# Kernel optimization log

Hardware: AMD Instinct MI355X
Metric: run time of the kernel (lower is better)

Reference implementation:

```python
import jax, jax.numpy as jnp
import numpy as np

N_HEAD, D_HEAD, D_MODEL = 16, 64, 1024
QLEN, MEMLEN, BSZ = 1024, 1024, 2
KLEN = QLEN + MEMLEN  # rlen == klen
LN_EPS = 1e-5
NEG = -1e30


def _rel_shift(x):
    # x: [qlen, rlen, bsz, n_head] -> Transformer-XL relative shift
    q, r, b, n = x.shape
    zp = jnp.zeros((q, 1, b, n), x.dtype)
    xp = jnp.concatenate([zp, x], axis=1).reshape(r + 1, q, b, n)
    return xp[1:].reshape(q, r, b, n)


def _layer_norm(x, gamma, beta):
    mu = jnp.mean(x, axis=-1, keepdims=True)
    var = jnp.mean((x - mu) ** 2, axis=-1, keepdims=True)
    return (x - mu) * jax.lax.rsqrt(var + LN_EPS) * gamma + beta


def setup_inputs() -> dict:
    key = jax.random.key(0)
    ks = jax.random.split(key, 8)
    w = jax.random.normal(ks[0], (QLEN, BSZ, D_MODEL), jnp.float32)
    r = jax.random.normal(ks[1], (KLEN, D_MODEL), jnp.float32)
    r_w_bias = jax.random.normal(ks[2], (N_HEAD, D_HEAD), jnp.float32) * 0.02
    r_r_bias = jax.random.normal(ks[3], (N_HEAD, D_HEAD), jnp.float32) * 0.02
    mems = jax.random.normal(ks[4], (MEMLEN, BSZ, D_MODEL), jnp.float32)
    W_qkv = jax.random.normal(ks[5], (D_MODEL, 3 * N_HEAD * D_HEAD), jnp.float32) * 0.02
    W_r = jax.random.normal(ks[6], (D_MODEL, N_HEAD * D_HEAD), jnp.float32) * 0.02
    W_o = jax.random.normal(ks[7], (N_HEAD * D_HEAD, D_MODEL), jnp.float32) * 0.02
    ln_gamma = jnp.ones((D_MODEL,), jnp.float32)
    ln_beta = jnp.zeros((D_MODEL,), jnp.float32)
    # causal mask with memory: key j visible to query i iff j <= i + MEMLEN (True = keep)
    attn_mask = jnp.arange(KLEN)[None, :] <= (jnp.arange(QLEN)[:, None] + MEMLEN)
    return {"w": w, "r": r, "r_w_bias": r_w_bias, "r_r_bias": r_r_bias,
            "mems": mems, "attn_mask": attn_mask, "W_qkv": W_qkv, "W_r": W_r,
            "W_o": W_o, "ln_gamma": ln_gamma, "ln_beta": ln_beta}


def reference(w, r, r_w_bias, r_r_bias, mems, attn_mask, W_qkv, W_r, W_o, ln_gamma, ln_beta):
    qlen, bsz = w.shape[0], w.shape[1]
    scale = 1.0 / (D_HEAD ** 0.5)
    cat = jnp.concatenate([mems, w], axis=0)            # [klen, b, d_model]
    klen = cat.shape[0]
    w_heads = cat @ W_qkv                                # [klen, b, 3*H*D]
    r_head_k = (r @ W_r).reshape(-1, N_HEAD, D_HEAD)     # [rlen, H, D]
    w_head_q, w_head_k, w_head_v = jnp.split(w_heads, 3, axis=-1)
    w_head_q = w_head_q[-qlen:].reshape(qlen, bsz, N_HEAD, D_HEAD)
    w_head_k = w_head_k.reshape(klen, bsz, N_HEAD, D_HEAD)
    w_head_v = w_head_v.reshape(klen, bsz, N_HEAD, D_HEAD)
    AC = jnp.einsum('ibnd,jbnd->ijbn', w_head_q + r_w_bias, w_head_k)
    BD = jnp.einsum('ibnd,jnd->ijbn', w_head_q + r_r_bias, r_head_k)
    BD = _rel_shift(BD)
    attn_score = (AC + BD) * scale                       # [q, k, b, n]
    attn_score = jnp.where(attn_mask[:, :, None, None], attn_score, NEG)
    attn_prob = jax.nn.softmax(attn_score, axis=1)
    attn_vec = jnp.einsum('ijbn,jbnd->ibnd', attn_prob, w_head_v)
    attn_vec = attn_vec.reshape(qlen, bsz, N_HEAD * D_HEAD)
    attn_out = attn_vec @ W_o                            # [q, b, d_model]
    return _layer_norm(w + attn_out, ln_gamma, ln_beta)
```

## Files before the change

kernel.cpp:

```cpp
#include <hip/hip_runtime.h>
#include <hip/hip_bf16.h>

#define NHEAD 16
#define DHEAD 64
#define DMODEL 1024
#define QLEN 1024
#define MEMLEN 1024
#define BSZ 2
#define KLEN 2048
#define LN_EPS 1e-5f

typedef __hip_bfloat16 bf16;
typedef __attribute__((ext_vector_type(8))) short short8;
typedef __attribute__((ext_vector_type(4))) float f32x4;

__device__ __forceinline__ float b2f(bf16 x) { return __bfloat162float(x); }
__device__ __forceinline__ bf16 f2b(float x) { return __float2bfloat16(x); }
__device__ __forceinline__ short f2bs(float f) {
    bf16 h = __float2bfloat16(f);
    return *reinterpret_cast<short*>(&h);
}
__device__ __forceinline__ float s2f(short s) {
    bf16 h = *reinterpret_cast<bf16*>(&s);
    return __bfloat162float(h);
}
__device__ __forceinline__ float fexp2(float x) {
    float y;
    asm("v_exp_f32 %0, %1" : "=v"(y) : "v"(x));
    return y;
}

#define MFMA16(a, b, c) __builtin_amdgcn_mfma_f32_16x16x32_bf16(a, b, c, 0, 0, 0)

#define AS1 __attribute__((address_space(1)))
#define AS3 __attribute__((address_space(3)))
__device__ __forceinline__ void gld16(const bf16* g, bf16* l) {
    __builtin_amdgcn_global_load_lds((const AS1 void*)(uintptr_t)g,
                                     (AS3 void*)(uint32_t)(uintptr_t)l, 16, 0, 0);
}

__global__ __launch_bounds__(256)
void prep(const float* __restrict__ mems, const float* __restrict__ w,
          const float* __restrict__ r, const float* __restrict__ Wqkv,
          const float* __restrict__ Wr, const float* __restrict__ Wo,
          bf16* __restrict__ Abf, bf16* __restrict__ rbf,
          bf16* __restrict__ Wqkvt, bf16* __restrict__ Wrt,
          bf16* __restrict__ Wot) {
    __shared__ bf16 T[64][65];
    const int id = blockIdx.x;
    const int t = threadIdx.x;
    if (id < 6144) {
        const float* src;
        bf16* dst;
        int off;
        if (id < 2048)      { src = mems; dst = Abf;                       off = id; }
        else if (id < 4096) { src = w;    dst = Abf + (size_t)2048 * 1024; off = id - 2048; }
        else                { src = r;    dst = rbf;                       off = id - 4096; }
        int i = off * 256 + t;
        const float4 v = reinterpret_cast<const float4*>(src)[i];
        bf16 o[4] = {f2b(v.x), f2b(v.y), f2b(v.z), f2b(v.w)};
        reinterpret_cast<ulong1*>(dst)[i] = *reinterpret_cast<ulong1*>(o);
        return;
    }
    int tid2 = id - 6144;
    const float* in;
    bf16* out;
    int N, tn, tile;
    if (tid2 < 768)       { in = Wqkv; out = Wqkvt; N = 3072; tn = 48; tile = tid2; }
    else if (tid2 < 1024) { in = Wr;   out = Wrt;   N = 1024; tn = 16; tile = tid2 - 768; }
    else                  { in = Wo;   out = Wot;   N = 1024; tn = 16; tile = tid2 - 1024; }
    const int K = 1024;
    const int n0 = (tile % tn) * 64, k0 = (tile / tn) * 64;
    #pragma unroll
    for (int e = 0; e < 16; e++) {
        int flat = e * 256 + t;
        int kl = flat >> 6, nl = flat & 63;
        T[kl][nl] = f2b(in[(size_t)(k0 + kl) * N + n0 + nl]);
    }
    __syncthreads();
    #pragma unroll
    for (int e = 0; e < 16; e++) {
        int flat = e * 256 + t;
        int nl = flat >> 6, kl = flat & 63;
        out[(size_t)(n0 + nl) * K + k0 + kl] = T[kl][nl];
    }
}

__global__ __launch_bounds__(256)
void gemm_mfma(const bf16* __restrict__ A, const bf16* __restrict__ Bt,
               const bf16* __restrict__ A2, const bf16* __restrict__ B2,
               int M, int N, int K, int mode,
               const float* __restrict__ rwb, const float* __restrict__ rrb,
               bf16* __restrict__ Qw, bf16* __restrict__ Qr,
               bf16* __restrict__ Kb, bf16* __restrict__ Vt,
               bf16* __restrict__ Cb, float* __restrict__ Cf,
               float* __restrict__ Cf2) {
    const int bm = blockIdx.x * 128, bn = blockIdx.y * 128;
    int sub = 0;
    const bf16* Ap = A;
    const bf16* Bp = Bt;
    if (mode == 0 && bm < 2048 && bn < 1024) { sub = 1; Ap = A2; Bp = B2; }
    const int ldk = (mode == 2) ? 1024 : K;
    float* Cfz = Cf;
    if (mode == 2 && blockIdx.z) { Ap += 512; Bp += 512; Cfz = Cf2; }
    __shared__ bf16 As[128 * 64];
    __shared__ bf16 Bs[128 * 64];
    const int t = threadIdx.x;
    const int w = t >> 6, lane = t & 63, quad = lane >> 4, l16 = lane & 15;
    const int wm = (w >> 1) * 64, wn = (w & 1) * 64;
    const int srow = lane >> 3;
    const int scs = ((lane & 7) ^ srow) * 8;
    const int c0 = (quad ^ (l16 & 7)) * 8;

    f32x4 acc[4][4];
    #pragma unroll
    for (int mt = 0; mt < 4; mt++)
        #pragma unroll
        for (int nt = 0; nt < 4; nt++) acc[mt][nt] = (f32x4){0.f, 0.f, 0.f, 0.f};

    for (int k0 = 0; k0 < K; k0 += 64) {
        #pragma unroll
        for (int e = 0; e < 4; e++) {
            int ch = w + 4 * e;
            int row = ch * 8 + srow;
            gld16(Ap + (size_t)(bm + row) * ldk + k0 + scs, As + ch * 512);
            gld16(Bp + (size_t)(bn + row) * ldk + k0 + scs, Bs + ch * 512);
        }
        __syncthreads();
        #pragma unroll
        for (int kk = 0; kk < 2; kk++) {
            const int cc = c0 ^ (kk << 5);
            short8 af[4], bfr[4];
            #pragma unroll
            for (int mt = 0; mt < 4; mt++)
                af[mt] = *reinterpret_cast<short8*>(&As[(wm + 16 * mt + l16) * 64 + cc]);
            #pragma unroll
            for (int nt = 0; nt < 4; nt++)
                bfr[nt] = *reinterpret_cast<short8*>(&Bs[(wn + 16 * nt + l16) * 64 + cc]);
            #pragma unroll
            for (int mt = 0; mt < 4; mt++)
                #pragma unroll
                for (int nt = 0; nt < 4; nt++)
                    acc[mt][nt] = MFMA16(af[mt], bfr[nt], acc[mt][nt]);
        }
        __syncthreads();
    }

    const float QSC = 0.18033688f;
    #pragma unroll
    for (int mt = 0; mt < 4; mt++)
        #pragma unroll
        for (int nt = 0; nt < 4; nt++)
            #pragma unroll
            for (int r = 0; r < 4; r++) {
                int m = bm + wm + 16 * mt + quad * 4 + r;
                int c = bn + wn + 16 * nt + l16;
                float v = acc[mt][nt][r];
                if (sub) {
                    Cb[(size_t)m * 1024 + c] = f2b(v);
                } else if (mode == 0) {
                    int seg = c >> 10, cc2 = c & 1023;
                    if (seg == 0) {
                        if (m >= 2048) {
                            size_t o = (size_t)(m - 2048) * 1024 + cc2;
                            Qw[o] = f2b((v + rwb[cc2]) * QSC);
                            Qr[o] = f2b((v + rrb[cc2]) * QSC);
                        }
                    } else if (seg == 1) {
                        Kb[(size_t)m * 1024 + cc2] = f2b(v);
                    } else {
                        Vt[((size_t)cc2 * 2 + (m & 1)) * 2048 + (m >> 1)] = f2b(v);
                    }
                } else {
                    Cfz[(size_t)m * N + c] = v;
                }
            }
}

__global__ __launch_bounds__(256, 3)
void attn_mfma(const bf16* __restrict__ Qw, const bf16* __restrict__ Qr,
               const bf16* __restrict__ Kb, const bf16* __restrict__ Vt,
               const bf16* __restrict__ Rk, float* __restrict__ O0g,
               float* __restrict__ O1g, float2* __restrict__ ML) {
    const int id = blockIdx.x;
    const int xcd = id & 7, local = id >> 3;
    const int pidx = local & 3;
    const int couple = (local >> 2) & 7;
    const int chunk = local >> 5;
    const int pair = xcd * 4 + pidx;
    const int b = pair & 1, n = pair >> 1;
    const int TA = couple + 17;
    const int t_beg = (chunk == 0) ? 0 : (chunk == 1) ? 17 : 33;
    const int t_end = (chunk == 0) ? 17 : (chunk == 1) ? 33 : 49;

    int segs[2][4];
    int nseg = 0;
    {
        int aend = min(t_end, TA);
        if (t_beg < aend) {
            segs[nseg][0] = couple; segs[nseg][1] = t_beg;
            segs[nseg][2] = aend;   segs[nseg][3] = (t_beg == 0) ? 0 : 1;
            nseg++;
        }
        int bbeg = max(t_beg, TA);
        if (bbeg < t_end) {
            segs[nseg][0] = 15 - couple; segs[nseg][1] = bbeg - TA;
            segs[nseg][2] = t_end - TA;  segs[nseg][3] = (bbeg == TA) ? 0 : 1;
            nseg++;
        }
    }

    const int tid = threadIdx.x;
    const int w = tid >> 6, lane = tid & 63;
    const int quad = lane >> 4, l16 = lane & 15;
    const int ln8 = lane >> 3;
    const int cs = (lane & 7) ^ (ln8 & 7);
    const int q0 = (quad ^ (l16 & 7)) * 8;
    const int q1 = q0 ^ 32;
    const int rbl = 48 - 16 * w;

    __shared__ bf16 Ks[64 * 64];
    __shared__ bf16 Vs[64 * 64];
    __shared__ bf16 Rs[3][64 * 64];
    __shared__ short WP_s[4][16 * 82];
    short* WP = WP_s[w];

    const int koff = b * 1024 + n * 64 + cs * 8;
    const size_t voff = (size_t)n * 262144 + b * 2048 + cs * 8;
    const int rcol = n * 64 + cs * 8;

    for (int sg = 0; sg < nseg; sg++) {
        const int i0 = segs[sg][0], jb = segs[sg][1], je = segs[sg][2], slot = segs[sg][3];
        const int I0 = i0 * 64;
        const int qbase = I0 + 16 * w;
        const int RB = 960 - I0;
        const int jlast = i0 + 16;

        auto stageKV = [&](int tt) {
            const int J0t = tt * 64;
            #pragma unroll
            for (int e = 0; e < 2; e++) {
                int ch = w + 4 * e;
                gld16(Vt + (size_t)(ch * 8 + ln8) * 4096 + voff + J0t, Vs + ch * 512);
                gld16(Kb + (size_t)(J0t + ch * 8 + ln8) * 2048 + koff, Ks + ch * 512);
            }
        };
        auto stageR = [&](int u) {
            bf16* rd = Rs[u % 3];
            #pragma unroll
            for (int e = 0; e < 2; e++) {
                int ch = w + 4 * e;
                int rrow = min(RB + u * 64 + ch * 8 + ln8, 2047);
                gld16(Rk + (size_t)rrow * 1024 + rcol, rd + ch * 512);
            }
        };

        short8 aqw[2], aqr[2];
        {
            const bf16* qp = Qw + ((size_t)(qbase + l16) * 2 + b) * 1024 + n * 64 + quad * 8;
            aqw[0] = *reinterpret_cast<const short8*>(qp);
            aqw[1] = *reinterpret_cast<const short8*>(qp + 32);
            const bf16* qp2 = Qr + ((size_t)(qbase + l16) * 2 + b) * 1024 + n * 64 + quad * 8;
            aqr[0] = *reinterpret_cast<const short8*>(qp2);
            aqr[1] = *reinterpret_cast<const short8*>(qp2 + 32);
        }

        f32x4 O[4];
        #pragma unroll
        for (int d = 0; d < 4; d++) O[d] = (f32x4){0.f, 0.f, 0.f, 0.f};
        float m_run = -1e30f;
        float pl[4] = {0.f, 0.f, 0.f, 0.f};

        if (sg) {
            asm volatile("s_waitcnt vmcnt(0)" ::: "memory");
            __builtin_amdgcn_s_barrier();
        }
        stageR(jb); stageR(jb + 1);

        for (int j = jb; j < je; j++) {
            const int J0 = j * 64;

            asm volatile("s_waitcnt vmcnt(0)" ::: "memory");
            __builtin_amdgcn_s_barrier();

            stageKV(j);
            stageR(j + 2);

            const bf16* R0 = Rs[j % 3];
            const bf16* R1 = Rs[(j + 1) % 3];

            #pragma unroll
            for (int s = 0; s < 5; s++) {
                int rb2 = rbl + 16 * s;
                const bf16* Rb = (rb2 & 64) ? R1 : R0;
                int rh = (rb2 & 63) + l16;
                short8 b0 = *reinterpret_cast<const short8*>(&Rb[rh * 64 + q0]);
                short8 b1 = *reinterpret_cast<const short8*>(&Rb[rh * 64 + q1]);
                f32x4 acc = (f32x4){0.f, 0.f, 0.f, 0.f};
                __builtin_amdgcn_s_setprio(1);
                acc = MFMA16(aqr[0], b0, acc);
                acc = MFMA16(aqr[1], b1, acc);
                __builtin_amdgcn_s_setprio(0);
                #pragma unroll
                for (int r = 0; r < 4; r++)
                    WP[(quad * 4 + r) * 82 + 16 * s + l16] = f2bs(acc[r]);
            }

            asm volatile("s_waitcnt vmcnt(2)" ::: "memory");
            __builtin_amdgcn_s_barrier();

            float sv[4][4];
            #pragma unroll
            for (int n16 = 0; n16 < 4; n16++) {
                int kr = 16 * n16 + l16;
                short8 k0 = *reinterpret_cast<const short8*>(&Ks[kr * 64 + q0]);
                short8 k1 = *reinterpret_cast<const short8*>(&Ks[kr * 64 + q1]);
                f32x4 acc = (f32x4){0.f, 0.f, 0.f, 0.f};
                __builtin_amdgcn_s_setprio(1);
                acc = MFMA16(aqw[0], k0, acc);
                acc = MFMA16(aqw[1], k1, acc);
                __builtin_amdgcn_s_setprio(0);
                #pragma unroll
                for (int r = 0; r < 4; r++) {
                    int row = quad * 4 + r, col = 16 * n16 + l16;
                    sv[n16][r] = acc[r] + s2f(WP[row * 82 + col - row + 15]);
                }
            }
            if (j == jlast) {
                #pragma unroll
                for (int n16 = 0; n16 < 4; n16++)
                    #pragma unroll
                    for (int r = 0; r < 4; r++) {
                        int row = quad * 4 + r, col = 16 * n16 + l16;
                        if (J0 + col > qbase + row + MEMLEN) sv[n16][r] = -1e30f;
                    }
            }

            float mx = sv[0][0];
            #pragma unroll
            for (int n16 = 0; n16 < 4; n16++)
                #pragma unroll
                for (int r = 0; r < 4; r++) mx = fmaxf(mx, sv[n16][r]);
            #pragma unroll
            for (int msk = 1; msk < 16; msk <<= 1) mx = fmaxf(mx, __shfl_xor(mx, msk));
            if (mx > m_run + 11.5f) {
                const float alpha = fexp2(m_run - mx);
                m_run = mx;
                #pragma unroll
                for (int r = 0; r < 4; r++) pl[r] *= alpha;
                #pragma unroll
                for (int d = 0; d < 4; d++)
                    #pragma unroll
                    for (int r = 0; r < 4; r++) O[d][r] *= alpha;
            }
            #pragma unroll
            for (int n16 = 0; n16 < 4; n16++)
                #pragma unroll
                for (int r = 0; r < 4; r++) sv[n16][r] = fexp2(sv[n16][r] - m_run);
            #pragma unroll
            for (int r = 0; r < 4; r++)
                pl[r] += sv[0][r] + sv[1][r] + sv[2][r] + sv[3][r];

            #pragma unroll
            for (int n16 = 0; n16 < 4; n16++)
                #pragma unroll
                for (int r = 0; r < 4; r++)
                    WP[(quad * 4 + r) * 72 + 16 * n16 + l16] = f2bs(sv[n16][r]);
            short8 ap0 = *reinterpret_cast<short8*>(&WP[l16 * 72 + quad * 8]);
            short8 ap1 = *reinterpret_cast<short8*>(&WP[l16 * 72 + 32 + quad * 8]);

            __builtin_amdgcn_s_setprio(1);
            #pragma unroll
            for (int ds = 0; ds < 4; ds++) {
                int dr = 16 * ds + l16;
                short8 v0 = *reinterpret_cast<const short8*>(&Vs[dr * 64 + q0]);
                short8 v1 = *reinterpret_cast<const short8*>(&Vs[dr * 64 + q1]);
                O[ds] = MFMA16(ap0, v0, O[ds]);
                O[ds] = MFMA16(ap1, v1, O[ds]);
            }
            __builtin_amdgcn_s_setprio(0);
        }

        float lr[4];
        #pragma unroll
        for (int r = 0; r < 4; r++) {
            float s = pl[r];
            #pragma unroll
            for (int msk = 1; msk < 16; msk <<= 1) s += __shfl_xor(s, msk);
            lr[r] = s;
        }
        if (l16 == 0) {
            #pragma unroll
            for (int r = 0; r < 4; r++) {
                int q = qbase + quad * 4 + r;
                ML[(size_t)slot * 32768 + (q * 2 + b) * 16 + n] =
                    make_float2(m_run, lr[r]);
            }
        }
        float* Od = slot ? O1g : O0g;
        #pragma unroll
        for (int ds = 0; ds < 4; ds++)
            #pragma unroll
            for (int r = 0; r < 4; r++) {
                int q = qbase + quad * 4 + r;
                Od[((size_t)q * 2 + b) * 1024 + n * 64 + 16 * ds + l16] = O[ds][r];
            }
    }
}

__global__ __launch_bounds__(256)
void attn_combine(const float* __restrict__ O0, const float* __restrict__ O1,
                  const float2* __restrict__ ML, bf16* __restrict__ AVbf) {
    const int row = blockIdx.x;
    const int t = threadIdx.x;
    const int n = t >> 4;
    const int i0 = row >> 7;
    const float2 a0 = ML[row * 16 + n];
    const f32x4 p0 = reinterpret_cast<const f32x4*>(O0)[row * 256 + t];
    short o[4];
    if (i0 != 0) {
        const float2 a1 = ML[32768 + row * 16 + n];
        const float m = fmaxf(a0.x, a1.x);
        const float e0 = fexp2(a0.x - m);
        const float e1 = fexp2(a1.x - m);
        const float inv = 1.f / (a0.y * e0 + a1.y * e1);
        const f32x4 p1 = reinterpret_cast<const f32x4*>(O1)[row * 256 + t];
        #pragma unroll
        for (int jj = 0; jj < 4; jj++)
            o[jj] = f2bs((p0[jj] * e0 + p1[jj] * e1) * inv);
    } else {
        const float inv = 1.f / a0.y;
        #pragma unroll
        for (int jj = 0; jj < 4; jj++) o[jj] = f2bs(p0[jj] * inv);
    }
    reinterpret_cast<ulong1*>(AVbf)[row * 256 + t] = *reinterpret_cast<ulong1*>(o);
}

__global__ __launch_bounds__(256)
void ln_res(const float* __restrict__ ao0, const float* __restrict__ ao1,
            const float* __restrict__ w, const float* __restrict__ gamma,
            const float* __restrict__ beta, float* __restrict__ out) {
    const int m = blockIdx.x;
    const int t = threadIdx.x;
    const int wv = t >> 6, lane = t & 63;
    __shared__ float red[8];
    float x[4];
    #pragma unroll
    for (int e = 0; e < 4; e++) {
        int c = e * 256 + t;
        x[e] = ao0[(size_t)m * DMODEL + c] + ao1[(size_t)m * DMODEL + c]
             + w[(size_t)m * DMODEL + c];
    }
    float s = x[0] + x[1] + x[2] + x[3];
    #pragma unroll
    for (int msk = 1; msk < 64; msk <<= 1) s += __shfl_xor(s, msk);
    if (lane == 0) red[wv] = s;
    __syncthreads();
    const float mu = (red[0] + red[1] + red[2] + red[3]) * (1.f / 1024.f);
    float s2 = 0.f;
    #pragma unroll
    for (int e = 0; e < 4; e++) { float dx = x[e] - mu; s2 += dx * dx; }
    #pragma unroll
    for (int msk = 1; msk < 64; msk <<= 1) s2 += __shfl_xor(s2, msk);
    if (lane == 0) red[4 + wv] = s2;
    __syncthreads();
    const float rstd = rsqrtf((red[4] + red[5] + red[6] + red[7]) * (1.f / 1024.f) + LN_EPS);
    #pragma unroll
    for (int e = 0; e < 4; e++) {
        int c = e * 256 + t;
        out[(size_t)m * DMODEL + c] = (x[e] - mu) * rstd * gamma[c] + beta[c];
    }
}

extern "C" void kernel_launch(void* const* d_in, const int* in_sizes, int n_in,
                              void* d_out, int out_size, void* d_ws, size_t ws_size,
                              hipStream_t stream) {
    const float* w        = (const float*)d_in[0];
    const float* r        = (const float*)d_in[1];
    const float* r_w_bias = (const float*)d_in[2];
    const float* r_r_bias = (const float*)d_in[3];
    const float* mems     = (const float*)d_in[4];
    const float* W_qkv    = (const float*)d_in[6];
    const float* W_r      = (const float*)d_in[7];
    const float* W_o      = (const float*)d_in[8];
    const float* gamma    = (const float*)d_in[9];
    const float* beta     = (const float*)d_in[10];
    float* out = (float*)d_out;

    bf16* Abf    = (bf16*)d_ws;
    bf16* Wqkvt  = Abf   + (size_t)4096 * 1024;
    bf16* Wrt    = Wqkvt + (size_t)3072 * 1024;
    bf16* Wot    = Wrt   + (size_t)1024 * 1024;
    bf16* rbf    = Wot   + (size_t)1024 * 1024;
    bf16* Qw     = rbf   + (size_t)2048 * 1024;
    bf16* Qr     = Qw    + (size_t)2048 * 1024;
    bf16* Kb     = Qr    + (size_t)2048 * 1024;
    bf16* Vt     = Kb    + (size_t)4096 * 1024;
    bf16* Rk     = Vt    + (size_t)2048 * 2048;
    bf16* AVbf   = Rk    + (size_t)2048 * 1024;
    float* Opart0   = (float*)Abf;
    float* Opart1   = (float*)Wqkvt;
    float2* ML      = (float2*)rbf;
    float* attn_out0 = (float*)Abf;
    float* attn_out1 = (float*)Wqkvt;

    dim3 b256(256);
    prep<<<dim3(7424), b256, 0, stream>>>(mems, w, r, W_qkv, W_r, W_o,
                                          Abf, rbf, Wqkvt, Wrt, Wot);
    gemm_mfma<<<dim3(32, 24), b256, 0, stream>>>(
        Abf, Wqkvt, rbf, Wrt, 4096, 3072, 1024, 0, r_w_bias, r_r_bias,
        Qw, Qr, Kb, Vt, Rk, nullptr, nullptr);
    attn_mfma<<<dim3(768), b256, 0, stream>>>(Qw, Qr, Kb, Vt, Rk,
                                              Opart0, Opart1, ML);
    attn_combine<<<dim3(2048), b256, 0, stream>>>(Opart0, Opart1, ML, AVbf);
    gemm_mfma<<<dim3(16, 8, 2), b256, 0, stream>>>(
        AVbf, Wot, nullptr, nullptr, 2048, 1024, 512, 2, nullptr, nullptr,
        nullptr, nullptr, nullptr, nullptr, nullptr, attn_out0, attn_out1);
    ln_res<<<dim3(QLEN * BSZ), b256, 0, stream>>>(attn_out0, attn_out1, w,
                                                  gamma, beta, out);
}
```

Measured before the change: 249.5 us.

## Double-buffer GEMM k-tiles and pre-tile V into MFMA fragment layout

The GEMM main loop now uses two 32-wide k-buffers in LDS, issuing the next tile's global loads before the MFMAs on the current tile, with one barrier per iteration instead of two. The QKV epilogue writes V directly in a pre-tiled layout that matches the attention kernel's MFMA B-fragment order. The attention kernel can then stage V as contiguous 4 KB blocks and read fragments with lane-linear, conflict-free LDS accesses. In exchange, the GEMM k-step is halved and the XOR swizzle is dropped, which may cause LDS bank conflicts on the A and B fragment reads. The V store from the epilogue also becomes more scattered.

Measured after the change: 242.2 us. 1.03x faster.

```diff
diff --git a/kernel.cpp b/kernel.cpp
--- a/kernel.cpp
+++ b/kernel.cpp
@@ -103,14 +103,22 @@
     const int ldk = (mode == 2) ? 1024 : K;
     float* Cfz = Cf;
     if (mode == 2 && blockIdx.z) { Ap += 512; Bp += 512; Cfz = Cf2; }
-    __shared__ bf16 As[128 * 64];
-    __shared__ bf16 Bs[128 * 64];
+    __shared__ bf16 As[2][128 * 32];
+    __shared__ bf16 Bs[2][128 * 32];
     const int t = threadIdx.x;
     const int w = t >> 6, lane = t & 63, quad = lane >> 4, l16 = lane & 15;
     const int wm = (w >> 1) * 64, wn = (w & 1) * 64;
-    const int srow = lane >> 3;
-    const int scs = ((lane & 7) ^ srow) * 8;
-    const int c0 = (quad ^ (l16 & 7)) * 8;
+    const int lrow = lane >> 2, lcol = (lane & 3) * 8;
+
+    auto stage = [&](int k0, int buf) {
+        #pragma unroll
+        for (int e = 0; e < 2; e++) {
+            int ch = w + 4 * e;
+            int row = ch * 16 + lrow;
+            gld16(Ap + (size_t)(bm + row) * ldk + k0 + lcol, As[buf] + ch * 512);
+            gld16(Bp + (size_t)(bn + row) * ldk + k0 + lcol, Bs[buf] + ch * 512);
+        }
+    };
 
     f32x4 acc[4][4];
     #pragma unroll
@@ -118,32 +126,26 @@
         #pragma unroll
         for (int nt = 0; nt < 4; nt++) acc[mt][nt] = (f32x4){0.f, 0.f, 0.f, 0.f};
 
-    for (int k0 = 0; k0 < K; k0 += 64) {
-        #pragma unroll
-        for (int e = 0; e < 4; e++) {
-            int ch = w + 4 * e;
-            int row = ch * 8 + srow;
-            gld16(Ap + (size_t)(bm + row) * ldk + k0 + scs, As + ch * 512);
-            gld16(Bp + (size_t)(bn + row) * ldk + k0 + scs, Bs + ch * 512);
-        }
-        __syncthreads();
-        #pragma unroll
-        for (int kk = 0; kk < 2; kk++) {
-            const int cc = c0 ^ (kk << 5);
-            short8 af[4], bfr[4];
-            #pragma unroll
-            for (int mt = 0; mt < 4; mt++)
-                af[mt] = *reinterpret_cast<short8*>(&As[(wm + 16 * mt + l16) * 64 + cc]);
+    stage(0, 0);
+    const int NK = K >> 5;
+    for (int kk = 0; kk < NK; kk++) {
+        asm volatile("s_waitcnt vmcnt(0)" ::: "memory");
+        __builtin_amdgcn_s_barrier();
+        if (kk + 1 < NK) stage((kk + 1) << 5, (kk + 1) & 1);
+        const bf16* A_ = As[kk & 1];
+        const bf16* B_ = Bs[kk & 1];
+        short8 af[4], bfr[4];
+        #pragma unroll
+        for (int mt = 0; mt < 4; mt++)
+            af[mt] = *reinterpret_cast<const short8*>(&A_[(wm + 16 * mt + l16) * 32 + quad * 8]);
+        #pragma unroll
+        for (int nt = 0; nt < 4; nt++)
+            bfr[nt] = *reinterpret_cast<const short8*>(&B_[(wn + 16 * nt + l16) * 32 + quad * 8]);
+        #pragma unroll
+        for (int mt = 0; mt < 4; mt++)
             #pragma unroll
             for (int nt = 0; nt < 4; nt++)
-                bfr[nt] = *reinterpret_cast<short8*>(&Bs[(wn + 16 * nt + l16) * 64 + cc]);
-            #pragma unroll
-            for (int mt = 0; mt < 4; mt++)
-                #pragma unroll
-                for (int nt = 0; nt < 4; nt++)
-                    acc[mt][nt] = MFMA16(af[mt], bfr[nt], acc[mt][nt]);
-        }
-        __syncthreads();
+                acc[mt][nt] = MFMA16(af[mt], bfr[nt], acc[mt][nt]);
     }
 
     const float QSC = 0.18033688f;
@@ -169,7 +171,14 @@
                     } else if (seg == 1) {
                         Kb[(size_t)m * 1024 + cc2] = f2b(v);
                     } else {
-                        Vt[((size_t)cc2 * 2 + (m & 1)) * 2048 + (m >> 1)] = f2b(v);
+                        int j = m >> 1, bb = m & 1;
+                        int vn = cc2 >> 6, dd = cc2 & 63;
+                        int ds = dd >> 4, l16v = dd & 15;
+                        int jt = j >> 6, jl = j & 63;
+                        int h = jl >> 5, qd = (jl >> 3) & 3, e = jl & 7;
+                        size_t addr = ((size_t)(vn * 2 + bb) * 32 + jt) * 4096
+                                    + (ds * 2 + h) * 512 + (qd * 16 + l16v) * 8 + e;
+                        Vt[addr] = f2b(v);
                     }
                 } else {
                     Cfz[(size_t)m * N + c] = v;
@@ -226,7 +235,7 @@
     short* WP = WP_s[w];
 
     const int koff = b * 1024 + n * 64 + cs * 8;
-    const size_t voff = (size_t)n * 262144 + b * 2048 + cs * 8;
+    const bf16* Vbase = Vt + (size_t)(n * 2 + b) * 131072 + lane * 8;
     const int rcol = n * 64 + cs * 8;
 
     for (int sg = 0; sg < nseg; sg++) {
@@ -238,10 +247,11 @@
 
         auto stageKV = [&](int tt) {
             const int J0t = tt * 64;
+            const bf16* vt = Vbase + (size_t)tt * 4096;
             #pragma unroll
             for (int e = 0; e < 2; e++) {
                 int ch = w + 4 * e;
-                gld16(Vt + (size_t)(ch * 8 + ln8) * 4096 + voff + J0t, Vs + ch * 512);
+                gld16(vt + ch * 512, Vs + ch * 512);
                 gld16(Kb + (size_t)(J0t + ch * 8 + ln8) * 2048 + koff, Ks + ch * 512);
             }
         };
@@ -372,9 +382,8 @@
             __builtin_amdgcn_s_setprio(1);
             #pragma unroll
             for (int ds = 0; ds < 4; ds++) {
-                int dr = 16 * ds + l16;
-                short8 v0 = *reinterpret_cast<const short8*>(&Vs[dr * 64 + q0]);
-                short8 v1 = *reinterpret_cast<const short8*>(&Vs[dr * 64 + q1]);
+                short8 v0 = *reinterpret_cast<const short8*>(&Vs[(ds * 2 + 0) * 512 + lane * 8]);
+                short8 v1 = *reinterpret_cast<const short8*>(&Vs[(ds * 2 + 1) * 512 + lane * 8]);
                 O[ds] = MFMA16(ap0, v0, O[ds]);
                 O[ds] = MFMA16(ap1, v1, O[ds]);
             }
```
